# Kernel tuning notes

Hardware: AMD Instinct MI355X
Metric: run time of the kernel (lower is better)

The kernel has to match this reference:

```python
import jax, jax.numpy as jnp
import numpy as np

B, C, H, W = 16, 128, 32, 32
D, K = 64, 8192
BN_EPS = 1e-5
KLD_SCALE = 10.0
COMMIT = 0.25


def setup_inputs() -> dict:
    key = jax.random.key(0)
    ks = jax.random.split(key, 4)
    return {
        "z": jax.random.normal(ks[0], (B, C, H, W), dtype=jnp.float32),
        "proj_w": jax.random.normal(ks[1], (D, C), dtype=jnp.float32) * (1.0 / np.sqrt(C)),
        "proj_b": jax.random.normal(ks[2], (D,), dtype=jnp.float32) * 0.01,
        "gamma": jnp.ones((D,), dtype=jnp.float32),
        "beta": jnp.zeros((D,), dtype=jnp.float32),
        "running_mean": jnp.zeros((D,), dtype=jnp.float32),
        "running_var": jnp.ones((D,), dtype=jnp.float32),
        "embed": jax.random.normal(ks[3], (K, D), dtype=jnp.float32) * 0.1,
    }


def reference(z, proj_w, proj_b, gamma, beta, running_mean, running_var, embed):
    sg = jax.lax.stop_gradient
    b, c, h, w = z.shape
    # 1x1 conv projection: [B,C,H,W] -> [B,D,H,W]
    x = jnp.einsum('bchw,dc->bdhw', z, proj_w) + proj_b[None, :, None, None]
    # BatchNorm2d (inference mode: running stats)
    scale = gamma * jax.lax.rsqrt(running_var + BN_EPS)
    x = x * scale[None, :, None, None] + (beta - running_mean * scale)[None, :, None, None]
    # NCHW -> NHWC, flatten to [N, D]
    z_e = jnp.transpose(x, (0, 2, 3, 1))
    flat = z_e.reshape(-1, z_e.shape[-1])  # [N, D]
    # pairwise squared distances [N, K]
    dist = (jnp.sum(flat * flat, axis=1, keepdims=True)
            - 2.0 * flat @ embed.T
            + jnp.sum(embed * embed, axis=1)[None, :])
    ind = jnp.argmax(-dist, axis=1).reshape(b, h, w)  # [B,H,W]
    z_q = embed[ind]  # [B,H,W,D] codebook gather
    diff = KLD_SCALE * (COMMIT * jnp.mean((sg(z_q) - z_e) ** 2)
                        + jnp.mean((z_q - sg(z_e)) ** 2))
    z_q_st = z_e + sg(z_q - z_e)  # straight-through
    return jnp.transpose(z_q_st, (0, 3, 1, 2)), diff, ind
```

## Files before the change

kernel.cpp:

```cpp
#include <hip/hip_runtime.h>
#include <math.h>

#define B_   16
#define C_   128
#define H_   32
#define W_   32
#define D_   64
#define K_   8192
#define HW_  (H_*W_)
#define N_   (B_*HW_)

#define CS      32
#define CPB     (K_/CS)
#define ROWS_PB 512
#define MARGIN  0.12f
#define CAND_CAP 32

typedef short v8s __attribute__((ext_vector_type(8)));
typedef float v4f __attribute__((ext_vector_type(4)));

__device__ __forceinline__ short f2bf(float f) {
    union { float fv; unsigned u; } cv; cv.fv = f;
    unsigned u = cv.u;
    unsigned rnd = ((u >> 16) & 1u) + 0x7fffu;
    return (short)((u + rnd) >> 16);
}

#define GLOAD_LDS16(gp, lp) __builtin_amdgcn_global_load_lds( \
    (const __attribute__((address_space(1))) unsigned int*)(gp), \
    (__attribute__((address_space(3))) unsigned int*)(lp), 16, 0, 0)

__device__ __forceinline__ float exact_score(const float4* __restrict__ zr,
                                             const float* __restrict__ embed,
                                             float h, int k)
{
    const float4* ep = (const float4*)(embed + (size_t)k * D_);
    float sa = 0.f, sb = 0.f;
    #pragma unroll
    for (int d4 = 0; d4 < 16; d4 += 2) {
        float4 ea = ep[d4], eb = ep[d4 + 1];
        sa += ea.x*zr[d4].x + ea.y*zr[d4].y + ea.z*zr[d4].z + ea.w*zr[d4].w;
        sb += eb.x*zr[d4+1].x + eb.y*zr[d4+1].y + eb.z*zr[d4+1].z + eb.w*zr[d4+1].w;
    }
    return (sa + sb) - h;
}

__global__ __launch_bounds__(256) void k_projprep(
    const float* __restrict__ z, const float* __restrict__ pw,
    const float* __restrict__ pb, const float* __restrict__ gamma,
    const float* __restrict__ beta, const float* __restrict__ rmean,
    const float* __restrict__ rvar, const float* __restrict__ embed,
    float* __restrict__ ze, short* __restrict__ zbfT,
    short* __restrict__ ebs, float* __restrict__ hn,
    int* __restrict__ cnt, float* __restrict__ outDiff)
{
    __shared__ float zt[128][64];
    __shared__ float wl[64][128];
    const int tid = threadIdx.x;

    if (blockIdx.x >= 256) {
        const int pbk = blockIdx.x - 256;
        int t = pbk * 256 + tid;
        float4 v = ((const float4*)embed)[t];
        float s = v.x*v.x + v.y*v.y + v.z*v.z + v.w*v.w;
        s += __shfl_xor(s, 1);
        s += __shfl_xor(s, 2);
        s += __shfl_xor(s, 4);
        s += __shfl_xor(s, 8);
        const int k = t >> 4, p = t & 15;
        if (p == 0) hn[k] = 0.5f * s;
        if (p < 8) {
            const int j = p ^ (k & 7);
            const float* src = embed + (size_t)k * D_ + j * 8;
            v8s o;
            #pragma unroll
            for (int i = 0; i < 8; ++i) o[i] = f2bf(src[i]);
            *(v8s*)(ebs + (size_t)k * D_ + p * 8) = o;
        }
        if (pbk < 64) cnt[pbk * 256 + tid] = 0;
        if (pbk == 0 && tid == 0) *outDiff = 0.f;
        return;
    }

    const int n0  = blockIdx.x * 64;
    const int b   = n0 / HW_;
    const int hw0 = n0 % HW_;
    const float* zb = z + (size_t)b * C_ * HW_ + hw0;

    #pragma unroll
    for (int it = 0; it < 8; ++it) {
        int flat = tid + 256 * it;
        int c = flat >> 4, p4 = flat & 15;
        *(float4*)&zt[c][4*p4] = *(const float4*)&zb[c * HW_ + 4*p4];
    }
    #pragma unroll
    for (int it = 0; it < 8; ++it) {
        int flat = tid + 256 * it;
        int d = flat >> 5, c4i = flat & 31;
        *(float4*)&wl[d][4*c4i] = *(const float4*)&pw[d * C_ + 4*c4i];
    }
    __syncthreads();

    const int tp = tid & 15;
    const int td = tid >> 4;
    float acc[4][4] = {};
    #pragma unroll
    for (int c4 = 0; c4 < 32; ++c4) {
        float4 zq[4], wv[4];
        #pragma unroll
        for (int k = 0; k < 4; ++k) zq[k] = *(const float4*)&zt[4*c4 + k][4*tp];
        #pragma unroll
        for (int j = 0; j < 4; ++j) wv[j] = *(const float4*)&wl[4*td + j][4*c4];
        #pragma unroll
        for (int i = 0; i < 4; ++i)
            #pragma unroll
            for (int j = 0; j < 4; ++j)
                acc[i][j] += zq[0][i]*wv[j].x + zq[1][i]*wv[j].y
                           + zq[2][i]*wv[j].z + zq[3][i]*wv[j].w;
    }

    float sc[4], bi[4];
    #pragma unroll
    for (int j = 0; j < 4; ++j) {
        int d = 4*td + j;
        float s = gamma[d] / sqrtf(rvar[d] + 1e-5f);
        sc[j] = s;
        bi[j] = pb[d] * s + beta[d] - rmean[d] * s;
    }
    short* tbase = zbfT + (size_t)blockIdx.x * 4096;
    const int islot_base = (tp >> 2) * 2 + (td >> 3);
    const int lane_hi    = ((td >> 1) & 3) * 16;
    const int el0        = 4 * (td & 1);
    #pragma unroll
    for (int i = 0; i < 4; ++i) {
        int n = n0 + 4*tp + i;
        float4 o;
        o.x = acc[i][0]*sc[0] + bi[0];
        o.y = acc[i][1]*sc[1] + bi[1];
        o.z = acc[i][2]*sc[2] + bi[2];
        o.w = acc[i][3]*sc[3] + bi[3];
        *(float4*)&ze[(size_t)n * D_ + 4*td] = o;
        short4 ob;
        ob.x = f2bf(o.x); ob.y = f2bf(o.y); ob.z = f2bf(o.z); ob.w = f2bf(o.w);
        const int lane = lane_hi + ((4*tp + i) & 15);
        *(short4*)(tbase + islot_base * 512 + lane * 8 + el0) = ob;
    }
}

template<bool PUSH>
__global__ __launch_bounds__(512) void k_sweep(
    const short* __restrict__ zbfT, const short* __restrict__ ebs,
    const float* __restrict__ hn, float* __restrict__ pbest,
    int* __restrict__ cnt, int* __restrict__ cand)
{
    __shared__ short eb[CPB * 64];
    __shared__ float hl[CPB];
    __shared__ float vml[ROWS_PB];
    const int tid  = threadIdx.x;
    const int lane = tid & 63;
    const int wv   = tid >> 6;
    const int q    = lane >> 4;
    const int l15  = lane & 15;
    const int m8   = l15 & 7;
    const int rowBase = blockIdx.x * ROWS_PB + wv * 64;
    const int code0   = blockIdx.y * CPB;

    {
        const char* s_ = (const char*)(ebs + (size_t)code0 * 64);
        char* l_ = (char*)&eb[0];
        #pragma unroll
        for (int i = 0; i < 4; ++i) {
            int seg = (wv * 4 + i) * 1024 + lane * 16;
            GLOAD_LDS16(s_ + seg, l_ + seg);
        }
        if (tid < CPB) hl[tid] = hn[code0 + tid];
    }

    if (PUSH) {
        float v = -INFINITY;
        const int row = blockIdx.x * ROWS_PB + tid;
        #pragma unroll
        for (int s = 0; s < CS; ++s) v = fmaxf(v, pbest[(size_t)s * N_ + row]);
        vml[tid] = v - MARGIN;
    }

    const short* aw = zbfT + (size_t)(blockIdx.x * 8 + wv) * 4096;
    v8s A[4][2];
    #pragma unroll
    for (int i = 0; i < 8; ++i)
        A[i >> 1][i & 1] = *(const v8s*)(aw + i * 512 + lane * 8);

    const int rb0 = l15 * 64 + ((q ^ m8) * 8);
    const int rb1 = l15 * 64 + (((q ^ m8) ^ 4) * 8);

    __syncthreads();

    float best[4][4];
    float vm[4][4];
    if (PUSH) {
        #pragma unroll
        for (int rt = 0; rt < 4; ++rt)
            #pragma unroll
            for (int r = 0; r < 4; ++r)
                vm[rt][r] = vml[wv * 64 + rt*16 + q*4 + r];
    } else {
        #pragma unroll
        for (int rt = 0; rt < 4; ++rt)
            #pragma unroll
            for (int r = 0; r < 4; ++r) best[rt][r] = -INFINITY;
    }

    #pragma unroll 1
    for (int tc = 0; tc < 2; ++tc) {
        #pragma unroll
        for (int ti = 0; ti < 8; ++ti) {
            const int t = tc * 8 + ti;
            v8s B0 = *(const v8s*)(&eb[0] + rb0 + t * 1024);
            v8s B1 = *(const v8s*)(&eb[0] + rb1 + t * 1024);
            const float mh = -hl[t * 16 + l15];
            #pragma unroll
            for (int rt = 0; rt < 4; ++rt) {
                v4f c = {mh, mh, mh, mh};
                c = __builtin_amdgcn_mfma_f32_16x16x32_bf16(A[rt][0], B0, c, 0, 0, 0);
                c = __builtin_amdgcn_mfma_f32_16x16x32_bf16(A[rt][1], B1, c, 0, 0, 0);
                if (!PUSH) {
                    #pragma unroll
                    for (int r = 0; r < 4; ++r) best[rt][r] = fmaxf(best[rt][r], c[r]);
                } else {
                    bool a0 = c[0] > vm[rt][0];
                    bool a1 = c[1] > vm[rt][1];
                    bool a2 = c[2] > vm[rt][2];
                    bool a3 = c[3] > vm[rt][3];
                    if (a0 | a1 | a2 | a3) {
                        const int code = code0 + t * 16 + l15;
                        const int row0 = rowBase + rt*16 + q*4;
                        #pragma unroll
                        for (int r = 0; r < 4; ++r) {
                            if (c[r] > vm[rt][r]) {
                                int s = atomicAdd(&cnt[row0 + r], 1);
                                if (s < CAND_CAP) cand[(row0 + r) * CAND_CAP + s] = code;
                            }
                        }
                    }
                }
            }
        }
    }

    if (!PUSH) {
        #pragma unroll
        for (int rt = 0; rt < 4; ++rt)
            #pragma unroll
            for (int r = 0; r < 4; ++r) {
                float v = best[rt][r];
                v = fmaxf(v, __shfl_xor(v, 1));
                v = fmaxf(v, __shfl_xor(v, 2));
                v = fmaxf(v, __shfl_xor(v, 4));
                v = fmaxf(v, __shfl_xor(v, 8));
                if (l15 == 0)
                    pbest[(size_t)blockIdx.y * N_ + rowBase + rt*16 + q*4 + r] = v;
            }
    }
}

__global__ __launch_bounds__(64) void k_pick(
    const int* __restrict__ cnt, const int* __restrict__ cand,
    const float* __restrict__ embed, const float* __restrict__ hn,
    const float* __restrict__ ze, float* __restrict__ out0,
    float* __restrict__ outIdx, float* __restrict__ outDiff)
{
    const int tid = threadIdx.x;
    const int n   = blockIdx.x * 64 + tid;

    float4 zr[16];
    const float4* zp = (const float4*)(ze + (size_t)n * D_);
    #pragma unroll
    for (int i = 0; i < 16; ++i) zr[i] = zp[i];

    const int m = cnt[n];
    float best = -INFINITY;
    int   bidx = 0x7fffffff;
    if (m == 0 || m > CAND_CAP) {
        for (int k = 0; k < K_; ++k) {
            float s = exact_score(zr, embed, hn[k], k);
            if (s > best) { best = s; bidx = k; }
        }
    } else {
        for (int i = 0; i < m; ++i) {
            int k = cand[n * CAND_CAP + i];
            float s = exact_score(zr, embed, hn[k], k);
            if (s > best || (s == best && k < bidx)) { best = s; bidx = k; }
        }
    }
    if (bidx == 0x7fffffff) bidx = 0;
    outIdx[n] = (float)bidx;

    const float4* eq = (const float4*)(embed + (size_t)bidx * D_);
    const int b = n >> 10, hw = n & 1023;
    float* o = out0 + (size_t)b * (D_ * HW_) + hw;

    float local = 0.f;
    #pragma unroll
    for (int d4 = 0; d4 < 16; ++d4) {
        float4 e = eq[d4], zv = zr[d4];
        float dx = e.x - zv.x, dy = e.y - zv.y, dz = e.z - zv.z, dw = e.w - zv.w;
        local += dx*dx + dy*dy + dz*dz + dw*dw;
        o[(4*d4 + 0) * HW_] = e.x;
        o[(4*d4 + 1) * HW_] = e.y;
        o[(4*d4 + 2) * HW_] = e.z;
        o[(4*d4 + 3) * HW_] = e.w;
    }

    local += __shfl_xor(local, 1);
    local += __shfl_xor(local, 2);
    local += __shfl_xor(local, 4);
    local += __shfl_xor(local, 8);
    local += __shfl_xor(local, 16);
    local += __shfl_xor(local, 32);
    if (tid == 0) atomicAdd(outDiff, local * (12.5f / (float)(N_ * D_)));
}

extern "C" void kernel_launch(void* const* d_in, const int* in_sizes, int n_in,
                              void* d_out, int out_size, void* d_ws, size_t ws_size,
                              hipStream_t stream)
{
    const float* z     = (const float*)d_in[0];
    const float* pw    = (const float*)d_in[1];
    const float* pb    = (const float*)d_in[2];
    const float* gamma = (const float*)d_in[3];
    const float* beta  = (const float*)d_in[4];
    const float* rmean = (const float*)d_in[5];
    const float* rvar  = (const float*)d_in[6];
    const float* embed = (const float*)d_in[7];

    float* out = (float*)d_out;
    float* out0    = out;
    float* outDiff = out + (size_t)N_ * D_;
    float* outIdx  = outDiff + 1;

    float* ws    = (float*)d_ws;
    float* ze    = ws;
    short* zbfT  = (short*)(ze + (size_t)N_ * D_);
    short* ebs   = zbfT + (size_t)N_ * D_;
    float* hn    = (float*)(ebs + (size_t)K_ * D_);
    float* pbest = hn + K_;
    int*   cnt   = (int*)(pbest + (size_t)CS * N_);
    int*   cand  = cnt + N_;

    k_projprep<<<256 + 512, 256, 0, stream>>>(z, pw, pb, gamma, beta, rmean,
                                              rvar, embed, ze, zbfT, ebs, hn,
                                              cnt, outDiff);
    k_sweep<false><<<dim3(N_ / ROWS_PB, CS), 512, 0, stream>>>(
        zbfT, ebs, hn, pbest, nullptr, nullptr);
    k_sweep<true><<<dim3(N_ / ROWS_PB, CS), 512, 0, stream>>>(
        zbfT, ebs, hn, pbest, cnt, cand);
    k_pick <<<N_ / 64, 64, 0, stream>>>(cnt, cand, embed, hn, ze, out0,
                                        outIdx, outDiff);
}
```

Measured before the change: 146.1 us.

## Fuse sweep, candidate push and pick into one per-row-block megakernel

Replaces the two full-grid sweep kernels and the separate pick kernel with one kernel. Each 64-row block streams the whole bf16 codebook twice through double-buffered LDS chunks: first to find the row maxima, then to push margin candidates into shared-memory lists. It then runs exact rescoring, the loss reduction and a coalesced transposed output write through LDS. This removes the per-split pbest global buffer, the global atomic candidate lists and two launches. In exchange every block rereads the entire codebook, there is a block barrier per chunk, and the pick stage uses only 8 lanes per wave.

```diff
diff --git a/kernel.cpp b/kernel.cpp
--- a/kernel.cpp
+++ b/kernel.cpp
@@ -10,10 +10,10 @@
 #define HW_  (H_*W_)
 #define N_   (B_*HW_)
 
-#define CS      32
-#define CPB     (K_/CS)
-#define ROWS_PB 512
-#define MARGIN  0.12f
+#define ROWS     64
+#define CHUNK    256
+#define NCH      (K_/CHUNK)
+#define MARGIN   0.12f
 #define CAND_CAP 32
 
 typedef short v8s __attribute__((ext_vector_type(8)));
@@ -52,7 +52,7 @@
     const float* __restrict__ rvar, const float* __restrict__ embed,
     float* __restrict__ ze, short* __restrict__ zbfT,
     short* __restrict__ ebs, float* __restrict__ hn,
-    int* __restrict__ cnt, float* __restrict__ outDiff)
+    float* __restrict__ outDiff)
 {
     __shared__ float zt[128][64];
     __shared__ float wl[64][128];
@@ -77,7 +77,6 @@
             for (int i = 0; i < 8; ++i) o[i] = f2bf(src[i]);
             *(v8s*)(ebs + (size_t)k * D_ + p * 8) = o;
         }
-        if (pbk < 64) cnt[pbk * 256 + tid] = 0;
         if (pbk == 0 && tid == 0) *outDiff = 0.f;
         return;
     }
@@ -147,177 +146,233 @@
     }
 }
 
-template<bool PUSH>
-__global__ __launch_bounds__(512) void k_sweep(
+__global__ __launch_bounds__(512) void k_megasweep(
     const short* __restrict__ zbfT, const short* __restrict__ ebs,
-    const float* __restrict__ hn, float* __restrict__ pbest,
-    int* __restrict__ cnt, int* __restrict__ cand)
+    const float* __restrict__ hn, const float* __restrict__ ze,
+    const float* __restrict__ embed, float* __restrict__ out0,
+    float* __restrict__ outIdx, float* __restrict__ outDiff)
 {
-    __shared__ short eb[CPB * 64];
-    __shared__ float hl[CPB];
-    __shared__ float vml[ROWS_PB];
+    __shared__ short EB[2][CHUNK * 64];
+    __shared__ float HL[2][CHUNK];
+    __shared__ float vpart[8][ROWS];
+    __shared__ float vml[ROWS];
+    __shared__ int   cntL[ROWS];
+    __shared__ int   candL[ROWS * CAND_CAP];
+    __shared__ int   bidxL[ROWS];
+    __shared__ float dpart[8];
+
     const int tid  = threadIdx.x;
     const int lane = tid & 63;
     const int wv   = tid >> 6;
     const int q    = lane >> 4;
     const int l15  = lane & 15;
     const int m8   = l15 & 7;
-    const int rowBase = blockIdx.x * ROWS_PB + wv * 64;
-    const int code0   = blockIdx.y * CPB;
-
-    {
-        const char* s_ = (const char*)(ebs + (size_t)code0 * 64);
-        char* l_ = (char*)&eb[0];
-        #pragma unroll
-        for (int i = 0; i < 4; ++i) {
-            int seg = (wv * 4 + i) * 1024 + lane * 16;
-            GLOAD_LDS16(s_ + seg, l_ + seg);
-        }
-        if (tid < CPB) hl[tid] = hn[code0 + tid];
-    }
-
-    if (PUSH) {
-        float v = -INFINITY;
-        const int row = blockIdx.x * ROWS_PB + tid;
-        #pragma unroll
-        for (int s = 0; s < CS; ++s) v = fmaxf(v, pbest[(size_t)s * N_ + row]);
-        vml[tid] = v - MARGIN;
-    }
-
-    const short* aw = zbfT + (size_t)(blockIdx.x * 8 + wv) * 4096;
+    const int bid  = blockIdx.x;
+    const int n0   = bid * ROWS;
+
+    const short* aw = zbfT + (size_t)bid * 4096;
     v8s A[4][2];
     #pragma unroll
     for (int i = 0; i < 8; ++i)
         A[i >> 1][i & 1] = *(const v8s*)(aw + i * 512 + lane * 8);
 
+    if (tid < ROWS) cntL[tid] = 0;
+
+    {
+        const char* s_ = (const char*)ebs;
+        char* l_ = (char*)&EB[0][0];
+        #pragma unroll
+        for (int i = 0; i < 4; ++i) {
+            int seg = i * 8192 + tid * 16;
+            GLOAD_LDS16(s_ + seg, l_ + seg);
+        }
+        if (tid < CHUNK) HL[0][tid] = hn[tid];
+    }
+
     const int rb0 = l15 * 64 + ((q ^ m8) * 8);
     const int rb1 = l15 * 64 + (((q ^ m8) ^ 4) * 8);
 
-    __syncthreads();
-
     float best[4][4];
     float vm[4][4];
-    if (PUSH) {
-        #pragma unroll
-        for (int rt = 0; rt < 4; ++rt)
-            #pragma unroll
-            for (int r = 0; r < 4; ++r)
-                vm[rt][r] = vml[wv * 64 + rt*16 + q*4 + r];
-    } else {
-        #pragma unroll
-        for (int rt = 0; rt < 4; ++rt)
-            #pragma unroll
-            for (int r = 0; r < 4; ++r) best[rt][r] = -INFINITY;
-    }
+    #pragma unroll
+    for (int rt = 0; rt < 4; ++rt)
+        #pragma unroll
+        for (int r = 0; r < 4; ++r) {
+            best[rt][r] = -INFINITY;
+            vm[rt][r]   = INFINITY;
+        }
+
+    __syncthreads();
 
     #pragma unroll 1
-    for (int tc = 0; tc < 2; ++tc) {
-        #pragma unroll
-        for (int ti = 0; ti < 8; ++ti) {
-            const int t = tc * 8 + ti;
-            v8s B0 = *(const v8s*)(&eb[0] + rb0 + t * 1024);
-            v8s B1 = *(const v8s*)(&eb[0] + rb1 + t * 1024);
-            const float mh = -hl[t * 16 + l15];
-            #pragma unroll
-            for (int rt = 0; rt < 4; ++rt) {
-                v4f c = {mh, mh, mh, mh};
-                c = __builtin_amdgcn_mfma_f32_16x16x32_bf16(A[rt][0], B0, c, 0, 0, 0);
-                c = __builtin_amdgcn_mfma_f32_16x16x32_bf16(A[rt][1], B1, c, 0, 0, 0);
-                if (!PUSH) {
+    for (int s = 0; s < 2 * NCH; ++s) {
+        const int cb = s & 1;
+        if (s < 2 * NCH - 1) {
+            const int nc = (s + 1) & (NCH - 1);
+            const char* s_ = (const char*)(ebs + (size_t)nc * (CHUNK * 64));
+            char* l_ = (char*)&EB[cb ^ 1][0];
+            #pragma unroll
+            for (int i = 0; i < 4; ++i) {
+                int seg = i * 8192 + tid * 16;
+                GLOAD_LDS16(s_ + seg, l_ + seg);
+            }
+            if (tid < CHUNK) HL[cb ^ 1][tid] = hn[nc * CHUNK + tid];
+        }
+        const short* ebp = &EB[cb][0];
+        const float* hlp = &HL[cb][0];
+
+        if (s < NCH) {
+            #pragma unroll
+            for (int ti = 0; ti < 2; ++ti) {
+                const int t = wv * 2 + ti;
+                v8s B0 = *(const v8s*)(ebp + rb0 + t * 1024);
+                v8s B1 = *(const v8s*)(ebp + rb1 + t * 1024);
+                const float mh = -hlp[t * 16 + l15];
+                #pragma unroll
+                for (int rt = 0; rt < 4; ++rt) {
+                    v4f c = {mh, mh, mh, mh};
+                    c = __builtin_amdgcn_mfma_f32_16x16x32_bf16(A[rt][0], B0, c, 0, 0, 0);
+                    c = __builtin_amdgcn_mfma_f32_16x16x32_bf16(A[rt][1], B1, c, 0, 0, 0);
                     #pragma unroll
                     for (int r = 0; r < 4; ++r) best[rt][r] = fmaxf(best[rt][r], c[r]);
-                } else {
+                }
+            }
+        } else {
+            const int codeBase = (s & (NCH - 1)) * CHUNK;
+            #pragma unroll
+            for (int ti = 0; ti < 2; ++ti) {
+                const int t = wv * 2 + ti;
+                v8s B0 = *(const v8s*)(ebp + rb0 + t * 1024);
+                v8s B1 = *(const v8s*)(ebp + rb1 + t * 1024);
+                const float mh = -hlp[t * 16 + l15];
+                #pragma unroll
+                for (int rt = 0; rt < 4; ++rt) {
+                    v4f c = {mh, mh, mh, mh};
+                    c = __builtin_amdgcn_mfma_f32_16x16x32_bf16(A[rt][0], B0, c, 0, 0, 0);
+                    c = __builtin_amdgcn_mfma_f32_16x16x32_bf16(A[rt][1], B1, c, 0, 0, 0);
                     bool a0 = c[0] > vm[rt][0];
                     bool a1 = c[1] > vm[rt][1];
                     bool a2 = c[2] > vm[rt][2];
                     bool a3 = c[3] > vm[rt][3];
                     if (a0 | a1 | a2 | a3) {
-                        const int code = code0 + t * 16 + l15;
-                        const int row0 = rowBase + rt*16 + q*4;
+                        const int code = codeBase + t * 16 + l15;
+                        const int row0 = rt * 16 + q * 4;
                         #pragma unroll
                         for (int r = 0; r < 4; ++r) {
                             if (c[r] > vm[rt][r]) {
-                                int s = atomicAdd(&cnt[row0 + r], 1);
-                                if (s < CAND_CAP) cand[(row0 + r) * CAND_CAP + s] = code;
+                                int sl = atomicAdd(&cntL[row0 + r], 1);
+                                if (sl < CAND_CAP) candL[(row0 + r) * CAND_CAP + sl] = code;
                             }
                         }
                     }
                 }
             }
         }
-    }
-
-    if (!PUSH) {
-        #pragma unroll
-        for (int rt = 0; rt < 4; ++rt)
-            #pragma unroll
-            for (int r = 0; r < 4; ++r) {
-                float v = best[rt][r];
-                v = fmaxf(v, __shfl_xor(v, 1));
-                v = fmaxf(v, __shfl_xor(v, 2));
-                v = fmaxf(v, __shfl_xor(v, 4));
-                v = fmaxf(v, __shfl_xor(v, 8));
-                if (l15 == 0)
-                    pbest[(size_t)blockIdx.y * N_ + rowBase + rt*16 + q*4 + r] = v;
-            }
-    }
-}
-
-__global__ __launch_bounds__(64) void k_pick(
-    const int* __restrict__ cnt, const int* __restrict__ cand,
-    const float* __restrict__ embed, const float* __restrict__ hn,
-    const float* __restrict__ ze, float* __restrict__ out0,
-    float* __restrict__ outIdx, float* __restrict__ outDiff)
-{
-    const int tid = threadIdx.x;
-    const int n   = blockIdx.x * 64 + tid;
-
-    float4 zr[16];
-    const float4* zp = (const float4*)(ze + (size_t)n * D_);
-    #pragma unroll
-    for (int i = 0; i < 16; ++i) zr[i] = zp[i];
-
-    const int m = cnt[n];
-    float best = -INFINITY;
-    int   bidx = 0x7fffffff;
-    if (m == 0 || m > CAND_CAP) {
-        for (int k = 0; k < K_; ++k) {
-            float s = exact_score(zr, embed, hn[k], k);
-            if (s > best) { best = s; bidx = k; }
-        }
-    } else {
-        for (int i = 0; i < m; ++i) {
-            int k = cand[n * CAND_CAP + i];
-            float s = exact_score(zr, embed, hn[k], k);
-            if (s > best || (s == best && k < bidx)) { best = s; bidx = k; }
-        }
-    }
-    if (bidx == 0x7fffffff) bidx = 0;
-    outIdx[n] = (float)bidx;
-
-    const float4* eq = (const float4*)(embed + (size_t)bidx * D_);
-    const int b = n >> 10, hw = n & 1023;
-    float* o = out0 + (size_t)b * (D_ * HW_) + hw;
-
-    float local = 0.f;
-    #pragma unroll
-    for (int d4 = 0; d4 < 16; ++d4) {
-        float4 e = eq[d4], zv = zr[d4];
-        float dx = e.x - zv.x, dy = e.y - zv.y, dz = e.z - zv.z, dw = e.w - zv.w;
-        local += dx*dx + dy*dy + dz*dz + dw*dw;
-        o[(4*d4 + 0) * HW_] = e.x;
-        o[(4*d4 + 1) * HW_] = e.y;
-        o[(4*d4 + 2) * HW_] = e.z;
-        o[(4*d4 + 3) * HW_] = e.w;
-    }
-
-    local += __shfl_xor(local, 1);
-    local += __shfl_xor(local, 2);
-    local += __shfl_xor(local, 4);
-    local += __shfl_xor(local, 8);
-    local += __shfl_xor(local, 16);
-    local += __shfl_xor(local, 32);
-    if (tid == 0) atomicAdd(outDiff, local * (12.5f / (float)(N_ * D_)));
+        __syncthreads();
+
+        if (s == NCH - 1) {
+            #pragma unroll
+            for (int rt = 0; rt < 4; ++rt)
+                #pragma unroll
+                for (int r = 0; r < 4; ++r) {
+                    float v = best[rt][r];
+                    v = fmaxf(v, __shfl_xor(v, 1));
+                    v = fmaxf(v, __shfl_xor(v, 2));
+                    v = fmaxf(v, __shfl_xor(v, 4));
+                    v = fmaxf(v, __shfl_xor(v, 8));
+                    if (l15 == 0) vpart[wv][rt * 16 + q * 4 + r] = v;
+                }
+            __syncthreads();
+            if (tid < ROWS) {
+                float v = vpart[0][tid];
+                #pragma unroll
+                for (int w = 1; w < 8; ++w) v = fmaxf(v, vpart[w][tid]);
+                vml[tid] = v - MARGIN;
+            }
+            __syncthreads();
+            #pragma unroll
+            for (int rt = 0; rt < 4; ++rt)
+                #pragma unroll
+                for (int r = 0; r < 4; ++r)
+                    vm[rt][r] = vml[rt * 16 + q * 4 + r];
+        }
+    }
+
+    if (lane < 8) {
+        const int r = wv * 8 + lane;
+        const int n = n0 + r;
+        float4 zr[16];
+        const float4* zp = (const float4*)(ze + (size_t)n * D_);
+        #pragma unroll
+        for (int i = 0; i < 16; ++i) zr[i] = zp[i];
+
+        const int m = cntL[r];
+        float bestv = -INFINITY;
+        int   bidx  = 0x7fffffff;
+        if (m == 0 || m > CAND_CAP) {
+            for (int k = 0; k < K_; ++k) {
+                float sc = exact_score(zr, embed, hn[k], k);
+                if (sc > bestv) { bestv = sc; bidx = k; }
+            }
+        } else {
+            for (int i = 0; i < m; ++i) {
+                int k = candL[r * CAND_CAP + i];
+                float sc = exact_score(zr, embed, hn[k], k);
+                if (sc > bestv || (sc == bestv && k < bidx)) { bestv = sc; bidx = k; }
+            }
+        }
+        if (bidx == 0x7fffffff) bidx = 0;
+        bidxL[r] = bidx;
+        outIdx[n] = (float)bidx;
+    }
+    __syncthreads();
+
+    float* zq = (float*)&EB[0][0];
+    {
+        const int r = tid >> 3, j = tid & 7;
+        const int bx = bidxL[r];
+        const float4* eq = (const float4*)(embed + (size_t)bx * D_ + j * 8);
+        float4 e0 = eq[0], e1 = eq[1];
+        const float4* zp = (const float4*)(ze + (size_t)(n0 + r) * D_ + j * 8);
+        float4 z0 = zp[0], z1 = zp[1];
+        float* zd = zq + r * 65 + j * 8;
+        zd[0] = e0.x; zd[1] = e0.y; zd[2] = e0.z; zd[3] = e0.w;
+        zd[4] = e1.x; zd[5] = e1.y; zd[6] = e1.z; zd[7] = e1.w;
+        float dx, local = 0.f;
+        dx = e0.x - z0.x; local += dx * dx;
+        dx = e0.y - z0.y; local += dx * dx;
+        dx = e0.z - z0.z; local += dx * dx;
+        dx = e0.w - z0.w; local += dx * dx;
+        dx = e1.x - z1.x; local += dx * dx;
+        dx = e1.y - z1.y; local += dx * dx;
+        dx = e1.z - z1.z; local += dx * dx;
+        dx = e1.w - z1.w; local += dx * dx;
+        local += __shfl_xor(local, 1);
+        local += __shfl_xor(local, 2);
+        local += __shfl_xor(local, 4);
+        local += __shfl_xor(local, 8);
+        local += __shfl_xor(local, 16);
+        local += __shfl_xor(local, 32);
+        if (lane == 0) dpart[wv] = local;
+    }
+    __syncthreads();
+    if (tid == 0) {
+        float v = 0.f;
+        #pragma unroll
+        for (int w = 0; w < 8; ++w) v += dpart[w];
+        atomicAdd(outDiff, v * (12.5f / (float)(N_ * D_)));
+    }
+
+    {
+        const int b = n0 >> 10, hw0 = n0 & 1023;
+        float* ob = out0 + (size_t)b * (D_ * HW_) + hw0;
+        #pragma unroll
+        for (int i = 0; i < 8; ++i) {
+            int flat = i * 512 + tid;
+            int d = flat >> 6, hh = flat & 63;
+            ob[d * HW_ + hh] = zq[hh * 65 + d];
+        }
+    }
 }
 
 extern "C" void kernel_launch(void* const* d_in, const int* in_sizes, int n_in,
@@ -343,17 +398,10 @@
     short* zbfT  = (short*)(ze + (size_t)N_ * D_);
     short* ebs   = zbfT + (size_t)N_ * D_;
     float* hn    = (float*)(ebs + (size_t)K_ * D_);
-    float* pbest = hn + K_;
-    int*   cnt   = (int*)(pbest + (size_t)CS * N_);
-    int*   cand  = cnt + N_;
 
     k_projprep<<<256 + 512, 256, 0, stream>>>(z, pw, pb, gamma, beta, rmean,
                                               rvar, embed, ze, zbfT, ebs, hn,
-                                              cnt, outDiff);
-    k_sweep<false><<<dim3(N_ / ROWS_PB, CS), 512, 0, stream>>>(
-        zbfT, ebs, hn, pbest, nullptr, nullptr);
-    k_sweep<true><<<dim3(N_ / ROWS_PB, CS), 512, 0, stream>>>(
-        zbfT, ebs, hn, pbest, cnt, cand);
-    k_pick <<<N_ / 64, 64, 0, stream>>>(cnt, cand, embed, hn, ze, out0,
-                                        outIdx, outDiff);
+                                              outDiff);
+    k_megasweep<<<N_ / ROWS, 512, 0, stream>>>(zbfT, ebs, hn, ze, embed,
+                                               out0, outIdx, outDiff);
 }
```

Result: slower. 171.2 us (+17.2%).

## Split candidate rescoring across four lanes per row and stage output via LDS

Applied to the files above, without the earlier changes.

The pick kernel now uses 256 threads per 64-row block. Each row's candidate (or fallback full) rescoring is split across four lanes, followed by a shuffle argmax reduction with index tie-break. The gathered codebook vectors are staged in a padded shared-memory tile and written to the NCHW output with coalesced stores, and the per-wave loss partials are reduced before one atomic. This removes serial per-thread candidate loops and the strided scattered stores, at the cost of extra synchronisation, shared memory, and reloading the z_e rows.

```diff
diff --git a/kernel.cpp b/kernel.cpp
--- a/kernel.cpp
+++ b/kernel.cpp
@@ -263,14 +263,23 @@
     }
 }
 
-__global__ __launch_bounds__(64) void k_pick(
+__global__ __launch_bounds__(256) void k_pick(
     const int* __restrict__ cnt, const int* __restrict__ cand,
     const float* __restrict__ embed, const float* __restrict__ hn,
     const float* __restrict__ ze, float* __restrict__ out0,
     float* __restrict__ outIdx, float* __restrict__ outDiff)
 {
-    const int tid = threadIdx.x;
-    const int n   = blockIdx.x * 64 + tid;
+    __shared__ float zqs[64 * 65];
+    __shared__ int   bidxL[64];
+    __shared__ float dpart[4];
+
+    const int tid  = threadIdx.x;
+    const int lane = tid & 63;
+    const int wv   = tid >> 6;
+    const int r    = tid >> 2;
+    const int slot = tid & 3;
+    const int n0   = blockIdx.x * 64;
+    const int n    = n0 + r;
 
     float4 zr[16];
     const float4* zp = (const float4*)(ze + (size_t)n * D_);
@@ -281,43 +290,67 @@
     float best = -INFINITY;
     int   bidx = 0x7fffffff;
     if (m == 0 || m > CAND_CAP) {
-        for (int k = 0; k < K_; ++k) {
+        for (int k = slot; k < K_; k += 4) {
             float s = exact_score(zr, embed, hn[k], k);
-            if (s > best) { best = s; bidx = k; }
+            if (s > best || (s == best && k < bidx)) { best = s; bidx = k; }
         }
     } else {
-        for (int i = 0; i < m; ++i) {
+        for (int i = slot; i < m; i += 4) {
             int k = cand[n * CAND_CAP + i];
             float s = exact_score(zr, embed, hn[k], k);
             if (s > best || (s == best && k < bidx)) { best = s; bidx = k; }
         }
     }
+    #pragma unroll
+    for (int d = 1; d < 4; d <<= 1) {
+        float ob = __shfl_xor(best, d);
+        int   oi = __shfl_xor(bidx, d);
+        if (ob > best || (ob == best && oi < bidx)) { best = ob; bidx = oi; }
+    }
     if (bidx == 0x7fffffff) bidx = 0;
-    outIdx[n] = (float)bidx;
-
-    const float4* eq = (const float4*)(embed + (size_t)bidx * D_);
-    const int b = n >> 10, hw = n & 1023;
-    float* o = out0 + (size_t)b * (D_ * HW_) + hw;
-
-    float local = 0.f;
-    #pragma unroll
-    for (int d4 = 0; d4 < 16; ++d4) {
-        float4 e = eq[d4], zv = zr[d4];
-        float dx = e.x - zv.x, dy = e.y - zv.y, dz = e.z - zv.z, dw = e.w - zv.w;
-        local += dx*dx + dy*dy + dz*dz + dw*dw;
-        o[(4*d4 + 0) * HW_] = e.x;
-        o[(4*d4 + 1) * HW_] = e.y;
-        o[(4*d4 + 2) * HW_] = e.z;
-        o[(4*d4 + 3) * HW_] = e.w;
-    }
-
-    local += __shfl_xor(local, 1);
-    local += __shfl_xor(local, 2);
-    local += __shfl_xor(local, 4);
-    local += __shfl_xor(local, 8);
-    local += __shfl_xor(local, 16);
-    local += __shfl_xor(local, 32);
-    if (tid == 0) atomicAdd(outDiff, local * (12.5f / (float)(N_ * D_)));
+    if (slot == 0) { bidxL[r] = bidx; outIdx[n] = (float)bidx; }
+    __syncthreads();
+
+    {
+        const int j  = slot;
+        const int bx = bidxL[r];
+        const float4* eq  = (const float4*)(embed + (size_t)bx * D_ + j * 16);
+        const float4* zp2 = (const float4*)(ze + (size_t)(n0 + r) * D_ + j * 16);
+        float* zd = zqs + r * 65 + j * 16;
+        float local = 0.f;
+        #pragma unroll
+        for (int t = 0; t < 4; ++t) {
+            float4 e = eq[t], zv = zp2[t];
+            zd[4*t + 0] = e.x; zd[4*t + 1] = e.y;
+            zd[4*t + 2] = e.z; zd[4*t + 3] = e.w;
+            float dx = e.x - zv.x, dy = e.y - zv.y;
+            float dz = e.z - zv.z, dw = e.w - zv.w;
+            local += dx*dx + dy*dy + dz*dz + dw*dw;
+        }
+        local += __shfl_xor(local, 1);
+        local += __shfl_xor(local, 2);
+        local += __shfl_xor(local, 4);
+        local += __shfl_xor(local, 8);
+        local += __shfl_xor(local, 16);
+        local += __shfl_xor(local, 32);
+        if (lane == 0) dpart[wv] = local;
+    }
+    __syncthreads();
+    if (tid == 0) {
+        float v = dpart[0] + dpart[1] + dpart[2] + dpart[3];
+        atomicAdd(outDiff, v * (12.5f / (float)(N_ * D_)));
+    }
+
+    {
+        const int b = n0 >> 10, hw0 = n0 & 1023;
+        float* ob = out0 + (size_t)b * (D_ * HW_) + hw0;
+        #pragma unroll
+        for (int i = 0; i < 16; ++i) {
+            int flat = i * 256 + tid;
+            int d = flat >> 6, hh = flat & 63;
+            ob[d * HW_ + hh] = zqs[hh * 65 + d];
+        }
+    }
 }
 
 extern "C" void kernel_launch(void* const* d_in, const int* in_sizes, int n_in,
@@ -354,6 +387,6 @@
         zbfT, ebs, hn, pbest, nullptr, nullptr);
     k_sweep<true><<<dim3(N_ / ROWS_PB, CS), 512, 0, stream>>>(
         zbfT, ebs, hn, pbest, cnt, cand);
-    k_pick <<<N_ / 64, 64, 0, stream>>>(cnt, cand, embed, hn, ze, out0,
+    k_pick<<<N_ / 64, 256, 0, stream>>>(cnt, cand, embed, hn, ze, out0,
                                         outIdx, outDiff);
 }
```

Measured after the change: 137.1 us. 6.2% less time.
